# Kernel optimization log

Hardware: AMD Instinct MI355X
Metric: run time of the kernel (lower is better)

The kernel has to match this reference:

```python
import jax, jax.numpy as jnp
import numpy as np

N_NODES = 100000
N_GRAPHS = 512
N_CHANNEL = 128
EPS = 0.001


def setup_inputs() -> dict:
    key = jax.random.key(0)
    k0, k1, k2, kb = jax.random.split(key, 4)
    x0 = jax.random.normal(k0, (N_NODES, N_CHANNEL), dtype=jnp.float32)
    x1 = jax.random.normal(k1, (N_NODES, N_CHANNEL, 3), dtype=jnp.float32)
    x2 = jax.random.normal(k2, (N_NODES, N_CHANNEL, 3, 3), dtype=jnp.float32)
    # sorted graph ids; guarantee every graph id appears at least once
    rest = jax.random.randint(kb, (N_NODES - N_GRAPHS,), 0, N_GRAPHS)
    batch = jnp.sort(jnp.concatenate([jnp.arange(N_GRAPHS), rest])).astype(jnp.int64)
    # degree = number of nodes per graph (matches the scatter divisor in torch code)
    degree = jax.ops.segment_sum(jnp.ones((N_NODES,), jnp.float32), batch,
                                 num_segments=N_GRAPHS)
    alpha = jnp.ones((3, N_CHANNEL), dtype=jnp.float32)
    beta = jnp.zeros((N_CHANNEL,), dtype=jnp.float32)
    gamma = jnp.ones((3, N_CHANNEL), dtype=jnp.float32)
    return {"x0": x0, "x1": x1, "x2": x2, "alpha": alpha, "beta": beta,
            "gamma": gamma, "batch": batch, "degree": degree}


def _norm_way(x, way, alpha_w, gamma_w, beta, batch, degree):
    # x: [N, C, 3^way...] ; per-graph mean/var over nodes via segment_sum
    deg = degree.reshape((-1,) + (1,) * (x.ndim - 1))          # [G,1,...]
    bcast = (1, -1) + (1,) * (x.ndim - 2)                      # [1,C,1,...]
    mean = jax.ops.segment_sum(x, batch, num_segments=N_GRAPHS) / deg
    x = x - mean[batch] * alpha_w.reshape(bcast)
    var = jax.ops.segment_sum(x * x, batch, num_segments=N_GRAPHS) / deg
    x = x / jnp.sqrt(var[batch] + EPS)
    x = x * gamma_w.reshape(bcast)
    if way == 0:
        x = x + beta[None, :]
    return x


def reference(x0, x1, x2, alpha, beta, gamma, batch, degree):
    out0 = _norm_way(x0, 0, alpha[0], gamma[0], beta, batch, degree)
    out1 = _norm_way(x1, 1, alpha[1], gamma[1], beta, batch, degree)
    out2 = _norm_way(x2, 2, alpha[2], gamma[2], beta, batch, degree)
    return (out0, out1, out2)
```

## Files before the change

kernel.cpp:

```cpp
#include <hip/hip_runtime.h>

#define NN 100000
#define NG 512
#define NCH 128
#define EPSV 0.001f
#define NCHUNK 52
#define NT 256
#define RCAP 10
#define OFF1 12800000L
#define OFF2 51200000L

__global__ void k_offsets(const int* __restrict__ b32, int* __restrict__ start) {
  int g = threadIdx.x;
  bool is64 = (b32[NN - 1] == 0);
  if (g < NG) {
    int lo = 0, hi = NN;
    while (lo < hi) {
      int mid = (lo + hi) >> 1;
      int v = is64 ? b32[2 * mid] : b32[mid];
      if (v < g) lo = mid + 1; else hi = mid;
    }
    start[g] = lo;
  }
  if (g == 0) start[NG] = NN;
}

__global__ __launch_bounds__(NT) void k_fused(
    const float* __restrict__ x0, const float* __restrict__ x1,
    const float* __restrict__ x2, const float* __restrict__ alpha,
    const float* __restrict__ beta, const float* __restrict__ gamma,
    const int* __restrict__ start, float* __restrict__ out) {
  int bid = blockIdx.x;
  int g = bid / NCHUNK;
  int k = bid - g * NCHUNK;

  const float* src; float* dst; int stride, cbase, gcomp0;
  if (k < 4)       { src = x0; dst = out;        stride = 128;  cbase = k * 32;      gcomp0 = cbase; }
  else if (k < 16) { src = x1; dst = out + OFF1; stride = 384;  cbase = (k-4) * 32;  gcomp0 = 128 + cbase; }
  else             { src = x2; dst = out + OFF2; stride = 1152; cbase = (k-16) * 32; gcomp0 = 512 + cbase; }

  int t  = threadIdx.x;
  int s  = t & 7;
  int ph = t >> 3;
  int ns = start[g], ne = start[g + 1];
  float invd = 1.0f / (float)(ne - ns);
  long coloff = (long)cbase + (s << 2);

  float s0=0,s1=0,s2=0,s3=0, q0=0,q1=0,q2=0,q3=0;
  float4 v[RCAP];
  #pragma unroll
  for (int i = 0; i < RCAP; ++i) {
    int n = ns + ph + (i << 5);
    if (n < ne) {
      float4 u = *reinterpret_cast<const float4*>(src + (long)n * stride + coloff);
      v[i] = u;
      s0 += u.x; s1 += u.y; s2 += u.z; s3 += u.w;
      q0 += u.x*u.x; q1 += u.y*u.y; q2 += u.z*u.z; q3 += u.w*u.w;
    }
  }
  for (int n = ns + ph + (RCAP << 5); n < ne; n += 32) {
    float4 u = *reinterpret_cast<const float4*>(src + (long)n * stride + coloff);
    s0 += u.x; s1 += u.y; s2 += u.z; s3 += u.w;
    q0 += u.x*u.x; q1 += u.y*u.y; q2 += u.z*u.z; q3 += u.w*u.w;
  }

  #define RED3(x) { x += __shfl_xor(x, 8); x += __shfl_xor(x, 16); x += __shfl_xor(x, 32); }
  RED3(s0) RED3(s1) RED3(s2) RED3(s3) RED3(q0) RED3(q1) RED3(q2) RED3(q3)
  #undef RED3

  __shared__ float red[4][8][8];
  int w = t >> 6, l = t & 63;
  if (l < 8) {
    red[w][l][0]=s0; red[w][l][1]=s1; red[w][l][2]=s2; red[w][l][3]=s3;
    red[w][l][4]=q0; red[w][l][5]=q1; red[w][l][6]=q2; red[w][l][7]=q3;
  }
  __syncthreads();

  float S[4], Q[4];
  #pragma unroll
  for (int j = 0; j < 4; ++j) {
    S[j] = red[0][s][j]   + red[1][s][j]   + red[2][s][j]   + red[3][s][j];
    Q[j] = red[0][s][j+4] + red[1][s][j+4] + red[2][s][j+4] + red[3][s][j+4];
  }

  float A[4], Bv[4], Be[4];
  #pragma unroll
  for (int j = 0; j < 4; ++j) {
    int c = gcomp0 + (s << 2) + j;
    int way, ch;
    if (c < 128)      { way = 0; ch = c; }
    else if (c < 512) { way = 1; ch = (c - 128) / 3; }
    else              { way = 2; ch = (c - 512) / 9; }
    float a  = alpha[way * NCH + ch];
    float gm = gamma[way * NCH + ch];
    float m  = S[j] * invd;
    float var = Q[j] * invd - m * m * a * (2.0f - a);
    A[j]  = m * a;
    Bv[j] = gm * rsqrtf(var + EPSV);
    Be[j] = (c < 128) ? beta[c] : 0.0f;
  }

  #pragma unroll
  for (int i = 0; i < RCAP; ++i) {
    int n = ns + ph + (i << 5);
    if (n < ne) {
      float4 u = v[i], o;
      o.x = (u.x - A[0]) * Bv[0] + Be[0];
      o.y = (u.y - A[1]) * Bv[1] + Be[1];
      o.z = (u.z - A[2]) * Bv[2] + Be[2];
      o.w = (u.w - A[3]) * Bv[3] + Be[3];
      *reinterpret_cast<float4*>(dst + (long)n * stride + coloff) = o;
    }
  }
  for (int n = ns + ph + (RCAP << 5); n < ne; n += 32) {
    float4 u = *reinterpret_cast<const float4*>(src + (long)n * stride + coloff);
    float4 o;
    o.x = (u.x - A[0]) * Bv[0] + Be[0];
    o.y = (u.y - A[1]) * Bv[1] + Be[1];
    o.z = (u.z - A[2]) * Bv[2] + Be[2];
    o.w = (u.w - A[3]) * Bv[3] + Be[3];
    *reinterpret_cast<float4*>(dst + (long)n * stride + coloff) = o;
  }
}

extern "C" void kernel_launch(void* const* d_in, const int* in_sizes, int n_in,
                              void* d_out, int out_size, void* d_ws, size_t ws_size,
                              hipStream_t stream) {
  const float* x0    = (const float*)d_in[0];
  const float* x1    = (const float*)d_in[1];
  const float* x2    = (const float*)d_in[2];
  const float* alpha = (const float*)d_in[3];
  const float* beta  = (const float*)d_in[4];
  const float* gamma = (const float*)d_in[5];
  const int*   b32   = (const int*)d_in[6];
  float* out = (float*)d_out;

  int* start = (int*)d_ws;

  k_offsets<<<1, 512, 0, stream>>>(b32, start);
  k_fused<<<NG * NCHUNK, NT, 0, stream>>>(x0, x1, x2, alpha, beta, gamma, start, out);
}
```

Measured before the change: 285.5 us.

## Widen column chunks to 64, use nontemporal loads/stores, template on stride

Each block now covers 64 columns with 16 node phases instead of 32 columns with 32 phases, which halves the block count and raises the register cache depth to 16 rows. Loads and stores use nontemporal builtins so the streamed data does not pollute the cache. The body is templated on the row stride so address math becomes compile-time constants. The deeper register cache may add register pressure and reduce occupancy, and 16-way node parallelism means more serial iterations per graph.

```diff
diff --git a/kernel.cpp b/kernel.cpp
--- a/kernel.cpp
+++ b/kernel.cpp
@@ -4,11 +4,13 @@
 #define NG 512
 #define NCH 128
 #define EPSV 0.001f
-#define NCHUNK 52
+#define NCHUNK 26
 #define NT 256
-#define RCAP 10
+#define RCAP 16
 #define OFF1 12800000L
 #define OFF2 51200000L
+
+typedef float f32x4 __attribute__((ext_vector_type(4)));
 
 __global__ void k_offsets(const int* __restrict__ b32, int* __restrict__ start) {
   int g = threadIdx.x;
@@ -25,52 +27,44 @@
   if (g == 0) start[NG] = NN;
 }
 
-__global__ __launch_bounds__(NT) void k_fused(
-    const float* __restrict__ x0, const float* __restrict__ x1,
-    const float* __restrict__ x2, const float* __restrict__ alpha,
-    const float* __restrict__ beta, const float* __restrict__ gamma,
-    const int* __restrict__ start, float* __restrict__ out) {
-  int bid = blockIdx.x;
-  int g = bid / NCHUNK;
-  int k = bid - g * NCHUNK;
-
-  const float* src; float* dst; int stride, cbase, gcomp0;
-  if (k < 4)       { src = x0; dst = out;        stride = 128;  cbase = k * 32;      gcomp0 = cbase; }
-  else if (k < 16) { src = x1; dst = out + OFF1; stride = 384;  cbase = (k-4) * 32;  gcomp0 = 128 + cbase; }
-  else             { src = x2; dst = out + OFF2; stride = 1152; cbase = (k-16) * 32; gcomp0 = 512 + cbase; }
-
+template<int STRIDE>
+static __device__ __forceinline__ void body(
+    const float* __restrict__ src, float* __restrict__ dst,
+    int cbase, int gcomp0,
+    const float* __restrict__ alpha, const float* __restrict__ beta,
+    const float* __restrict__ gamma, int ns, int ne,
+    float (*red)[16][8]) {
   int t  = threadIdx.x;
-  int s  = t & 7;
-  int ph = t >> 3;
-  int ns = start[g], ne = start[g + 1];
+  int s  = t & 15;
+  int ph = t >> 4;
   float invd = 1.0f / (float)(ne - ns);
   long coloff = (long)cbase + (s << 2);
+  const float* p0 = src + (long)(ns + ph) * STRIDE + coloff;
 
   float s0=0,s1=0,s2=0,s3=0, q0=0,q1=0,q2=0,q3=0;
-  float4 v[RCAP];
+  f32x4 v[RCAP];
   #pragma unroll
   for (int i = 0; i < RCAP; ++i) {
-    int n = ns + ph + (i << 5);
-    if (n < ne) {
-      float4 u = *reinterpret_cast<const float4*>(src + (long)n * stride + coloff);
+    if (ns + ph + (i << 4) < ne) {
+      f32x4 u = __builtin_nontemporal_load(
+          reinterpret_cast<const f32x4*>(p0 + (long)i * 16 * STRIDE));
       v[i] = u;
       s0 += u.x; s1 += u.y; s2 += u.z; s3 += u.w;
       q0 += u.x*u.x; q1 += u.y*u.y; q2 += u.z*u.z; q3 += u.w*u.w;
     }
   }
-  for (int n = ns + ph + (RCAP << 5); n < ne; n += 32) {
-    float4 u = *reinterpret_cast<const float4*>(src + (long)n * stride + coloff);
+  for (int n = ns + ph + (RCAP << 4); n < ne; n += 16) {
+    f32x4 u = __builtin_nontemporal_load(
+        reinterpret_cast<const f32x4*>(src + (long)n * STRIDE + coloff));
     s0 += u.x; s1 += u.y; s2 += u.z; s3 += u.w;
     q0 += u.x*u.x; q1 += u.y*u.y; q2 += u.z*u.z; q3 += u.w*u.w;
   }
 
-  #define RED3(x) { x += __shfl_xor(x, 8); x += __shfl_xor(x, 16); x += __shfl_xor(x, 32); }
-  RED3(s0) RED3(s1) RED3(s2) RED3(s3) RED3(q0) RED3(q1) RED3(q2) RED3(q3)
-  #undef RED3
-
-  __shared__ float red[4][8][8];
+  #define RED2(x) { x += __shfl_xor(x, 16); x += __shfl_xor(x, 32); }
+  RED2(s0) RED2(s1) RED2(s2) RED2(s3) RED2(q0) RED2(q1) RED2(q2) RED2(q3)
+  #undef RED2
   int w = t >> 6, l = t & 63;
-  if (l < 8) {
+  if (l < 16) {
     red[w][l][0]=s0; red[w][l][1]=s1; red[w][l][2]=s2; red[w][l][3]=s3;
     red[w][l][4]=q0; red[w][l][5]=q1; red[w][l][6]=q2; red[w][l][7]=q3;
   }
@@ -100,27 +94,51 @@
     Be[j] = (c < 128) ? beta[c] : 0.0f;
   }
 
+  float* q0p = dst + (long)(ns + ph) * STRIDE + coloff;
   #pragma unroll
   for (int i = 0; i < RCAP; ++i) {
-    int n = ns + ph + (i << 5);
-    if (n < ne) {
-      float4 u = v[i], o;
+    if (ns + ph + (i << 4) < ne) {
+      f32x4 u = v[i], o;
       o.x = (u.x - A[0]) * Bv[0] + Be[0];
       o.y = (u.y - A[1]) * Bv[1] + Be[1];
       o.z = (u.z - A[2]) * Bv[2] + Be[2];
       o.w = (u.w - A[3]) * Bv[3] + Be[3];
-      *reinterpret_cast<float4*>(dst + (long)n * stride + coloff) = o;
+      __builtin_nontemporal_store(o,
+          reinterpret_cast<f32x4*>(q0p + (long)i * 16 * STRIDE));
     }
   }
-  for (int n = ns + ph + (RCAP << 5); n < ne; n += 32) {
-    float4 u = *reinterpret_cast<const float4*>(src + (long)n * stride + coloff);
-    float4 o;
+  for (int n = ns + ph + (RCAP << 4); n < ne; n += 16) {
+    f32x4 u = __builtin_nontemporal_load(
+        reinterpret_cast<const f32x4*>(src + (long)n * STRIDE + coloff));
+    f32x4 o;
     o.x = (u.x - A[0]) * Bv[0] + Be[0];
     o.y = (u.y - A[1]) * Bv[1] + Be[1];
     o.z = (u.z - A[2]) * Bv[2] + Be[2];
     o.w = (u.w - A[3]) * Bv[3] + Be[3];
-    *reinterpret_cast<float4*>(dst + (long)n * stride + coloff) = o;
+    __builtin_nontemporal_store(o,
+        reinterpret_cast<f32x4*>(dst + (long)n * STRIDE + coloff));
   }
+}
+
+__global__ __launch_bounds__(NT) void k_fused(
+    const float* __restrict__ x0, const float* __restrict__ x1,
+    const float* __restrict__ x2, const float* __restrict__ alpha,
+    const float* __restrict__ beta, const float* __restrict__ gamma,
+    const int* __restrict__ start, float* __restrict__ out) {
+  __shared__ float red[4][16][8];
+  int bid = blockIdx.x;
+  int g = bid / NCHUNK;
+  int k = bid - g * NCHUNK;
+  int ns = start[g], ne = start[g + 1];
+
+  if (k < 2)
+    body<128>(x0, out, k * 64, k * 64, alpha, beta, gamma, ns, ne, red);
+  else if (k < 8)
+    body<384>(x1, out + OFF1, (k - 2) * 64, 128 + (k - 2) * 64,
+              alpha, beta, gamma, ns, ne, red);
+  else
+    body<1152>(x2, out + OFF2, (k - 8) * 64, 512 + (k - 8) * 64,
+               alpha, beta, gamma, ns, ne, red);
 }
 
 extern "C" void kernel_launch(void* const* d_in, const int* in_sizes, int n_in,
```

Measured after the change: 242.7 us. -15.0%, faster.
